# Kernel tuning notes

Measured on AMD Instinct MI355X. Metric: run time of the kernel, lower is better.

The kernel has to match this reference:

```python
import jax, jax.numpy as jnp
import numpy as np

# SectorAttention (PARTNER): dim=256, resolution=(4,4096), H_sp=4, W_sp=1, H=4, heads=8
B, Hq, Hres, Wres, C, NH = 4, 4, 4, 4096, 256, 8
H_SP, W_SP = 4, 1
HD = C // NH
SCALE = HD ** -0.5


def _forward(s, x, s_pos, x_pos, Wq, bq, Wk, bk, Wv, bv, Wo, bo,
             pw1, pb1, bn_g, bn_b, bn_m, bn_v, pw2, pb2,
             ln_g, ln_b, mw1, mb1, mw2, mb2):
    Bb, Lq, Cc = s.shape
    W = Wres
    nW = Bb * (W // W_SP)
    # ---- dynamic relative-position bias (per-window small conv net) ----
    xp = x_pos.reshape(Bb, Hq // H_SP, H_SP, W // W_SP, W_SP, 2)
    xp = jnp.transpose(xp, (0, 1, 3, 5, 2, 4)).reshape(-1, 2, H_SP * W_SP)   # (nW,2,4)
    sp = jnp.transpose(s_pos, (0, 2, 3, 1)).reshape(-1, 2, Hq * W_SP)        # (nW,2,4)
    rel = sp[:, :, :, None] - xp[:, :, None, :]                              # (nW,2,4,4)
    rel = rel.reshape(nW, 2, -1)                                             # (nW,2,16)
    h = jnp.einsum('oc,bcl->bol', pw1, rel) + pb1[None, :, None]             # Conv1d k=1
    h = (h - bn_m[None, :, None]) * jax.lax.rsqrt(bn_v[None, :, None] + 1e-5) \
        * bn_g[None, :, None] + bn_b[None, :, None]                          # BatchNorm1d (eval)
    h = jax.nn.relu(h)
    h = jnp.einsum('oc,bcl->bol', pw2, h) + pb2[None, :, None]               # Conv1d k=1 -> heads
    rel_bias = h.reshape(-1, NH, Hq, H_SP)                                   # (nW,NH,4,4) since W_SP==1
    # ---- projections + window partitioning ----
    q = s @ Wq.T + bq
    q = q.reshape(Bb, Cc, Hq, W)                          # faithful torch .view reinterpretation
    q = q.reshape(Bb, NH, HD, Hq, W // W_SP, W_SP)
    q = jnp.transpose(q, (0, 4, 1, 3, 5, 2)).reshape(-1, NH, Hq * W_SP, HD)

    def im2cswin(t):
        t = jnp.transpose(t, (0, 2, 1)).reshape(Bb, Cc, Hres, W)
        t = t.reshape(Bb, Cc, Hres // H_SP, H_SP, W // W_SP, W_SP)
        t = jnp.transpose(t, (0, 2, 4, 3, 5, 1)).reshape(-1, H_SP * W_SP, Cc)
        return jnp.transpose(t.reshape(-1, H_SP * W_SP, NH, HD), (0, 2, 1, 3))

    k = im2cswin(x @ Wk.T + bk)
    v = im2cswin(x @ Wv.T + bv)
    # ---- windowed attention with dynamic bias ----
    attn = jnp.einsum('wnqd,wnkd->wnqk', q * SCALE, k) + rel_bias
    attn = jax.nn.softmax(attn, axis=-1)
    o = jnp.einsum('wnqk,wnkd->wnqd', attn, v)            # (nW,NH,4,HD)
    o = jnp.transpose(o, (0, 2, 1, 3)).reshape(-1, Hq * W_SP, Cc)
    # windows2img(o, H_sp=Hq, W_sp=W_SP, H=Hq, W=W)
    o = o.reshape(Bb, Hq // Hq, W // W_SP, Hq, W_SP, Cc)
    o = jnp.transpose(o, (0, 1, 3, 2, 4, 5)).reshape(Bb, Hq * W, Cc)
    o = o @ Wo.T + bo
    s1 = s + o
    # ---- LayerNorm + MLP (residual) ----
    mu = jnp.mean(s1, axis=-1, keepdims=True)
    var = jnp.mean((s1 - mu) ** 2, axis=-1, keepdims=True)
    n = (s1 - mu) * jax.lax.rsqrt(var + 1e-5) * ln_g + ln_b
    h2 = jax.nn.gelu(n @ mw1.T + mb1, approximate=False)
    return s1 + h2 @ mw2.T + mb2


def setup_inputs() -> dict:
    key = jax.random.key(0)
    ks = jax.random.split(key, 12)
    rn = lambda k, sh, sc=1.0: jax.random.normal(k, sh, dtype=jnp.float32) * sc
    H4 = 4 * C
    return {
        's': rn(ks[0], (B, Hq * Wres, C)),
        'x': rn(ks[1], (B, Hres * Wres, C)),
        's_pos': rn(ks[2], (B, 2, Wres // W_SP, Hq * W_SP)),
        'x_pos': rn(ks[3], (B, Hres * Wres, 2)),
        'Wq': rn(ks[4], (C, C), 0.02), 'bq': jnp.zeros((C,), jnp.float32),
        'Wk': rn(ks[5], (C, C), 0.02), 'bk': jnp.zeros((C,), jnp.float32),
        'Wv': rn(ks[6], (C, C), 0.02), 'bv': jnp.zeros((C,), jnp.float32),
        'Wo': rn(ks[7], (C, C), 0.02), 'bo': jnp.zeros((C,), jnp.float32),
        'pw1': rn(ks[8], (16, 2), 0.2), 'pb1': jnp.zeros((16,), jnp.float32),
        'bn_g': jnp.ones((16,), jnp.float32), 'bn_b': jnp.zeros((16,), jnp.float32),
        'bn_m': jnp.zeros((16,), jnp.float32), 'bn_v': jnp.ones((16,), jnp.float32),
        'pw2': rn(ks[9], (NH, 16), 0.2), 'pb2': jnp.zeros((NH,), jnp.float32),
        'ln_g': jnp.ones((C,), jnp.float32), 'ln_b': jnp.zeros((C,), jnp.float32),
        'mw1': rn(ks[10], (H4, C), 0.02), 'mb1': jnp.zeros((H4,), jnp.float32),
        'mw2': rn(ks[11], (C, H4), 0.02), 'mb2': jnp.zeros((C,), jnp.float32),
    }


def reference(s, x, s_pos, x_pos, Wq, bq, Wk, bk, Wv, bv, Wo, bo,
              pw1, pb1, bn_g, bn_b, bn_m, bn_v, pw2, pb2,
              ln_g, ln_b, mw1, mb1, mw2, mb2):
    return _forward(s, x, s_pos, x_pos, Wq, bq, Wk, bk, Wv, bv, Wo, bo,
                    pw1, pb1, bn_g, bn_b, bn_m, bn_v, pw2, pb2,
                    ln_g, ln_b, mw1, mb1, mw2, mb2)
```

## Files before the change

### kernel.cpp

```cpp
#include <hip/hip_runtime.h>
#include <hip/hip_bf16.h>
#include <math.h>

typedef __hip_bfloat16 BF;
typedef __bf16 bf16x8 __attribute__((ext_vector_type(8)));
typedef float f32x4 __attribute__((ext_vector_type(4)));

struct alignas(8) BF4 { BF v[4]; };
struct alignas(16) BF8 { BF v[8]; };

static __device__ __forceinline__ float b2f(BF x) { return __bfloat162float(x); }
static __device__ __forceinline__ BF f2b(float x) { return __float2bfloat16(x); }

static __device__ __forceinline__ void gld_lds16(const void* g, void* l) {
  __builtin_amdgcn_global_load_lds(
      (const __attribute__((address_space(1))) unsigned int*)g,
      (__attribute__((address_space(3))) unsigned int*)l, 16, 0, 0);
}

__global__ void __launch_bounds__(256) cvt_kernel(
    const float* __restrict__ in, BF* __restrict__ out, int n4) {
  for (int i = blockIdx.x * 256 + threadIdx.x; i < n4; i += gridDim.x * 256) {
    float4 v = ((const float4*)in)[i];
    BF4 o;
    o.v[0] = f2b(v.x); o.v[1] = f2b(v.y); o.v[2] = f2b(v.z); o.v[3] = f2b(v.w);
    ((BF4*)out)[i] = o;
  }
}

__global__ void __launch_bounds__(256) bkv_kernel(
    const float* __restrict__ bk, const float* __restrict__ bv,
    float* __restrict__ bkv) {
  int i = blockIdx.x * 256 + threadIdx.x;
  bkv[i] = (i < 256) ? bk[i] : bv[i - 256];
}

__global__ void __launch_bounds__(256) bias_kernel(
    const float* __restrict__ s_pos, const float* __restrict__ x_pos,
    const float* __restrict__ pw1, const float* __restrict__ pb1,
    const float* __restrict__ bn_g, const float* __restrict__ bn_b,
    const float* __restrict__ bn_m, const float* __restrict__ bn_v,
    const float* __restrict__ pw2, const float* __restrict__ pb2,
    float* __restrict__ out) {
  int gid = blockIdx.x * 256 + threadIdx.x;
  int w = gid >> 4, l = gid & 15;
  int b = w >> 12, wi = w & 4095;
  int i = l >> 2, j = l & 3;
  int e0 = i, e1 = 4 + i;
  float sp0 = s_pos[(((size_t)b * 2 + (e0 & 1)) * 4096 + wi) * 4 + (e0 >> 1)];
  float sp1 = s_pos[(((size_t)b * 2 + (e1 & 1)) * 4096 + wi) * 4 + (e1 >> 1)];
  float xp0 = x_pos[((size_t)b * 16384 + j * 4096 + wi) * 2 + 0];
  float xp1 = x_pos[((size_t)b * 16384 + j * 4096 + wi) * 2 + 1];
  float r0 = sp0 - xp0, r1 = sp1 - xp1;
  float acc[8];
#pragma unroll
  for (int p = 0; p < 8; ++p) acc[p] = pb2[p];
#pragma unroll
  for (int o = 0; o < 16; ++o) {
    float t = pw1[o * 2 + 0] * r0 + pw1[o * 2 + 1] * r1 + pb1[o];
    float sc = bn_g[o] / sqrtf(bn_v[o] + 1e-5f);
    t = (t - bn_m[o]) * sc + bn_b[o];
    t = fmaxf(t, 0.0f);
#pragma unroll
    for (int p = 0; p < 8; ++p) acc[p] += pw2[p * 16 + o] * t;
  }
#pragma unroll
  for (int p = 0; p < 8; ++p) out[(size_t)w * 128 + p * 16 + l] = acc[p];
}

enum { EPI_NONE = 0, EPI_RES = 1, EPI_GELU = 2 };

template <int EPI, typename AT, typename RT, typename CT>
__global__ void __launch_bounds__(256, 4) gemm_tn(
    const AT* __restrict__ A, const BF* __restrict__ Bw,
    const float* __restrict__ bias, const RT* __restrict__ Res,
    CT* __restrict__ C, int M, int N, int K) {
  constexpr bool F32A = __is_same(AT, float);
  alignas(16) __shared__ BF As[8][128][8];
  alignas(16) __shared__ BF Bs[8][128][8];
  const int ntiles = N >> 7;
  const int cpx = gridDim.x >> 3;
  const int bid = blockIdx.x;
  const int swz = (bid & 7) * cpx + (bid >> 3);
  const int mt = swz / ntiles, nt = swz % ntiles;
  const int row0 = mt << 7, col0 = nt << 7;
  const int t = threadIdx.x;
  const int wave = t >> 6, lane = t & 63;
  const int wr = wave >> 1, wc = wave & 1;
  const int sm = t & 127;
  const int skc = t >> 7;
  f32x4 acc[4][4] = {};
  const int NT = K >> 6;
  float4 ar[4][2];

  auto stageB = [&](int kt) {
#pragma unroll
    for (int i = 0; i < 4; ++i) {
      const int kc = i * 2 + skc;
      gld_lds16(Bw + (size_t)(col0 + sm) * K + kt * 64 + kc * 8,
                &Bs[0][0][0] + (size_t)(i * 256 + wave * 64) * 8);
    }
  };
  auto loadA = [&](int kt) {
    if constexpr (F32A) {
#pragma unroll
      for (int i = 0; i < 4; ++i) {
        const int kc = i * 2 + skc;
        const float* src = A + (size_t)(row0 + sm) * K + kt * 64 + kc * 8;
        ar[i][0] = ((const float4*)src)[0];
        ar[i][1] = ((const float4*)src)[1];
      }
    }
  };
  auto writeA = [&]() {
    if constexpr (F32A) {
#pragma unroll
      for (int i = 0; i < 4; ++i) {
        const int kc = i * 2 + skc;
        BF tmp[8];
        tmp[0] = f2b(ar[i][0].x); tmp[1] = f2b(ar[i][0].y);
        tmp[2] = f2b(ar[i][0].z); tmp[3] = f2b(ar[i][0].w);
        tmp[4] = f2b(ar[i][1].x); tmp[5] = f2b(ar[i][1].y);
        tmp[6] = f2b(ar[i][1].z); tmp[7] = f2b(ar[i][1].w);
        *(bf16x8*)(&As[kc][sm][0]) = *(bf16x8*)tmp;
      }
    }
  };
  auto stageA_bf = [&](int kt) {
    if constexpr (!F32A) {
#pragma unroll
      for (int i = 0; i < 4; ++i) {
        const int kc = i * 2 + skc;
        gld_lds16((const BF*)A + (size_t)(row0 + sm) * K + kt * 64 + kc * 8,
                  &As[0][0][0] + (size_t)(i * 256 + wave * 64) * 8);
      }
    }
  };
  auto compute = [&]() {
#pragma unroll
    for (int kk = 0; kk < 2; ++kk) {
      const int chunk = kk * 4 + (lane >> 4);
      const int rl = lane & 15;
      bf16x8 af[4], bfr[4];
#pragma unroll
      for (int mi = 0; mi < 4; ++mi)
        af[mi] = *(const bf16x8*)(&As[chunk][wr * 64 + mi * 16 + rl][0]);
#pragma unroll
      for (int ni = 0; ni < 4; ++ni)
        bfr[ni] = *(const bf16x8*)(&Bs[chunk][wc * 64 + ni * 16 + rl][0]);
#pragma unroll
      for (int mi = 0; mi < 4; ++mi)
#pragma unroll
        for (int ni = 0; ni < 4; ++ni)
          acc[mi][ni] = __builtin_amdgcn_mfma_f32_16x16x32_bf16(
              af[mi], bfr[ni], acc[mi][ni], 0, 0, 0);
    }
  };

  loadA(0);
  for (int kt = 0; kt < NT; ++kt) {
    writeA();
    stageA_bf(kt);
    stageB(kt);
    if (kt + 1 < NT) loadA(kt + 1);
    __syncthreads();
    compute();
    __syncthreads();
  }

  const int rl = lane & 15, rg = lane >> 4;
#pragma unroll
  for (int mi = 0; mi < 4; ++mi) {
#pragma unroll
    for (int ni = 0; ni < 4; ++ni) {
      const int col = col0 + wc * 64 + ni * 16 + rl;
      const float bcol = bias[col];
#pragma unroll
      for (int r = 0; r < 4; ++r) {
        const int row = row0 + wr * 64 + mi * 16 + rg * 4 + r;
        float v = acc[mi][ni][r] + bcol;
        if constexpr (EPI == EPI_GELU)
          v = 0.5f * v * (1.0f + erff(v * 0.70710678118654752f));
        if constexpr (EPI == EPI_RES) {
          if constexpr (__is_same(RT, float))
            v += Res[(size_t)row * N + col];
          else
            v += b2f(Res[(size_t)row * N + col]);
        }
        if constexpr (__is_same(CT, float))
          C[(size_t)row * N + col] = v;
        else
          C[(size_t)row * N + col] = f2b(v);
      }
    }
  }
}

__global__ void __launch_bounds__(256, 4) gemm_q(
    const float* __restrict__ A, const BF* __restrict__ Bw,
    const float* __restrict__ bias, BF* __restrict__ Qa) {
  constexpr int K = 256;
  alignas(16) __shared__ BF As[8][128][8];
  alignas(16) __shared__ BF Bs[8][128][8];
  const int cpx = gridDim.x >> 3;
  const int bid = blockIdx.x;
  const int swz = (bid & 7) * cpx + (bid >> 3);
  const int mt = swz >> 1, nt = swz & 1;
  const int hp = mt & 3, qi = (mt >> 2) & 3, nh = (mt >> 4) & 7, bb = mt >> 7;
  const int col0 = nt << 7;
  const int t = threadIdx.x;
  const int wave = t >> 6, lane = t & 63;
  const int wr = wave >> 1, wc = wave & 1;
  const int sm = t & 127;
  const int skc = t >> 7;
  const size_t grow = (size_t)bb * 16384 + nh * 2048 + (size_t)(sm & 31) * 64 +
                      qi * 16 + hp * 4 + (sm >> 5);
  f32x4 acc[4][4] = {};
  float4 ar[4][2];

  auto stageB = [&](int kt) {
#pragma unroll
    for (int i = 0; i < 4; ++i) {
      const int kc = i * 2 + skc;
      gld_lds16(Bw + (size_t)(col0 + sm) * K + kt * 64 + kc * 8,
                &Bs[0][0][0] + (size_t)(i * 256 + wave * 64) * 8);
    }
  };
  auto loadA = [&](int kt) {
#pragma unroll
    for (int i = 0; i < 4; ++i) {
      const int kc = i * 2 + skc;
      const float* src = A + grow * K + kt * 64 + kc * 8;
      ar[i][0] = ((const float4*)src)[0];
      ar[i][1] = ((const float4*)src)[1];
    }
  };
  auto writeA = [&]() {
#pragma unroll
    for (int i = 0; i < 4; ++i) {
      const int kc = i * 2 + skc;
      BF tmp[8];
      tmp[0] = f2b(ar[i][0].x); tmp[1] = f2b(ar[i][0].y);
      tmp[2] = f2b(ar[i][0].z); tmp[3] = f2b(ar[i][0].w);
      tmp[4] = f2b(ar[i][1].x); tmp[5] = f2b(ar[i][1].y);
      tmp[6] = f2b(ar[i][1].z); tmp[7] = f2b(ar[i][1].w);
      *(bf16x8*)(&As[kc][sm][0]) = *(bf16x8*)tmp;
    }
  };
  auto compute = [&]() {
#pragma unroll
    for (int kk = 0; kk < 2; ++kk) {
      const int chunk = kk * 4 + (lane >> 4);
      const int rl = lane & 15;
      bf16x8 af[4], bfr[4];
#pragma unroll
      for (int mi = 0; mi < 4; ++mi)
        af[mi] = *(const bf16x8*)(&As[chunk][wr * 64 + mi * 16 + rl][0]);
#pragma unroll
      for (int ni = 0; ni < 4; ++ni)
        bfr[ni] = *(const bf16x8*)(&Bs[chunk][wc * 64 + ni * 16 + rl][0]);
#pragma unroll
      for (int mi = 0; mi < 4; ++mi)
#pragma unroll
        for (int ni = 0; ni < 4; ++ni)
          acc[mi][ni] = __builtin_amdgcn_mfma_f32_16x16x32_bf16(
              af[mi], bfr[ni], acc[mi][ni], 0, 0, 0);
    }
  };

  loadA(0);
  for (int kt = 0; kt < 4; ++kt) {
    writeA();
    stageB(kt);
    if (kt + 1 < 4) loadA(kt + 1);
    __syncthreads();
    compute();
    __syncthreads();
  }

  const int rl = lane & 15, rg = lane >> 4;
  const float SCALE = 0.17677669529663689f;
#pragma unroll
  for (int mi = 0; mi < 4; ++mi) {
#pragma unroll
    for (int ni = 0; ni < 4; ++ni) {
      const int col = col0 + wc * 64 + ni * 16 + rl;
      const float bcol = bias[col];
      const int i0 = wr * 64 + mi * 16 + rg * 4;
      const int hd = i0 & 31, hil = i0 >> 5;
      const int wi = (hp * 4 + hil) * 256 + col;
      BF4 pk;
#pragma unroll
      for (int r = 0; r < 4; ++r)
        pk.v[r] = f2b((acc[mi][ni][r] + bcol) * SCALE);
      *(BF4*)(Qa + ((((size_t)bb * 4096 + wi) * 8 + nh) * 128 + qi * 32 + hd)) = pk;
    }
  }
}

__global__ void __launch_bounds__(256) attn_kernel(
    const BF* __restrict__ Qa, const BF* __restrict__ KV,
    const float* __restrict__ biasb, BF* __restrict__ O) {
  const int t = threadIdx.x;
  const int g = t >> 4, l16 = t & 15;
  const int qi = l16 >> 2, kj = l16 & 3;
  const int w = (blockIdx.x << 1) | (g >> 3);
  const int nh = g & 7;
  const int b = w >> 12, wi = w & 4095;

  const uint4* qp = (const uint4*)(Qa + ((((size_t)b * 4096 + wi) * 8 + nh) * 128 + qi * 32));
  uint4 qv[4] = {qp[0], qp[1], qp[2], qp[3]};
  const uint4* kp = (const uint4*)(KV + ((size_t)b * 16384 + kj * 4096 + wi) * 512 + nh * 32);
  uint4 kv[4] = {kp[0], kp[1], kp[2], kp[3]};
  const float bias_l = biasb[(size_t)w * 128 + nh * 16 + l16];
  const BF* vbase = KV + (size_t)b * 16384 * 512 + 256 + nh * 32 + kj * 8;
  uint4 vv[4];
#pragma unroll
  for (int d = 0; d < 4; ++d)
    vv[d] = *(const uint4*)(vbase + ((size_t)((kj ^ d) * 4096 + wi)) * 512);

  float accs[4] = {0.f, 0.f, 0.f, 0.f};
#pragma unroll
  for (int j = 0; j < 4; ++j) {
#pragma unroll
    for (int e = 0; e < 4; ++e) {
      unsigned qe = ((const unsigned*)&qv[j])[e];
      unsigned ke = ((const unsigned*)&kv[j])[e];
      float ql = __uint_as_float(qe << 16);
      float qh = __uint_as_float(qe & 0xffff0000u);
      float kl = __uint_as_float(ke << 16);
      float kh = __uint_as_float(ke & 0xffff0000u);
      accs[e] = fmaf(ql, kl, accs[e]);
      accs[e] = fmaf(qh, kh, accs[e]);
    }
  }
  const float score = accs[0] + accs[1] + accs[2] + accs[3] + bias_l;

  float mx = fmaxf(score, __shfl_xor(score, 1));
  mx = fmaxf(mx, __shfl_xor(mx, 2));
  float e = __expf(score - mx);
  float sm = e + __shfl_xor(e, 1);
  sm += __shfl_xor(sm, 2);
  float p = e / sm;
  float pd[4];
  pd[0] = p;
  pd[1] = __shfl_xor(p, 1);
  pd[2] = __shfl_xor(p, 2);
  pd[3] = __shfl_xor(pd[1], 2);

  float o8[8] = {0.f, 0.f, 0.f, 0.f, 0.f, 0.f, 0.f, 0.f};
#pragma unroll
  for (int d = 0; d < 4; ++d) {
#pragma unroll
    for (int e2 = 0; e2 < 4; ++e2) {
      unsigned ve = ((const unsigned*)&vv[d])[e2];
      o8[e2 * 2 + 0] = fmaf(pd[d], __uint_as_float(ve << 16), o8[e2 * 2 + 0]);
      o8[e2 * 2 + 1] = fmaf(pd[d], __uint_as_float(ve & 0xffff0000u), o8[e2 * 2 + 1]);
    }
  }
  BF8 ob;
#pragma unroll
  for (int h = 0; h < 8; ++h) ob.v[h] = f2b(o8[h]);
  *(BF8*)(O + ((size_t)b * 16384 + qi * 4096 + wi) * 256 + nh * 32 + kj * 8) = ob;
}

__global__ void __launch_bounds__(256) ln_kernel(
    const BF* __restrict__ S1, const float* __restrict__ g,
    const float* __restrict__ be, BF* __restrict__ Nout) {
  const int wave = threadIdx.x >> 6, lane = threadIdx.x & 63;
  const size_t row = (size_t)blockIdx.x * 4 + wave;
  BF4 d = *(const BF4*)(S1 + row * 256 + lane * 4);
  float x[4] = {b2f(d.v[0]), b2f(d.v[1]), b2f(d.v[2]), b2f(d.v[3])};
  float s = x[0] + x[1] + x[2] + x[3];
  float sq = x[0] * x[0] + x[1] * x[1] + x[2] * x[2] + x[3] * x[3];
#pragma unroll
  for (int m = 1; m <= 32; m <<= 1) {
    s += __shfl_xor(s, m);
    sq += __shfl_xor(sq, m);
  }
  const float mean = s * 0.00390625f;
  const float var = sq * 0.00390625f - mean * mean;
  const float rstd = 1.0f / sqrtf(var + 1e-5f);
  BF4 o;
#pragma unroll
  for (int jj = 0; jj < 4; ++jj) {
    float nv = (x[jj] - mean) * rstd * g[lane * 4 + jj] + be[lane * 4 + jj];
    o.v[jj] = f2b(nv);
  }
  *(BF4*)(Nout + row * 256 + lane * 4) = o;
}

extern "C" void kernel_launch(void* const* d_in, const int* in_sizes, int n_in,
                              void* d_out, int out_size, void* d_ws, size_t ws_size,
                              hipStream_t stream) {
  const float* s     = (const float*)d_in[0];
  const float* x     = (const float*)d_in[1];
  const float* s_pos = (const float*)d_in[2];
  const float* x_pos = (const float*)d_in[3];
  const float* Wq = (const float*)d_in[4];  const float* bq = (const float*)d_in[5];
  const float* Wk = (const float*)d_in[6];  const float* bk = (const float*)d_in[7];
  const float* Wv = (const float*)d_in[8];  const float* bv = (const float*)d_in[9];
  const float* Wo = (const float*)d_in[10]; const float* bo = (const float*)d_in[11];
  const float* pw1 = (const float*)d_in[12]; const float* pb1 = (const float*)d_in[13];
  const float* bn_g = (const float*)d_in[14]; const float* bn_b = (const float*)d_in[15];
  const float* bn_m = (const float*)d_in[16]; const float* bn_v = (const float*)d_in[17];
  const float* pw2 = (const float*)d_in[18]; const float* pb2 = (const float*)d_in[19];
  const float* ln_g = (const float*)d_in[20]; const float* ln_b = (const float*)d_in[21];
  const float* mw1 = (const float*)d_in[22]; const float* mb1 = (const float*)d_in[23];
  const float* mw2 = (const float*)d_in[24]; const float* mb2 = (const float*)d_in[25];

  char* ws = (char*)d_ws;
  float* biasb = (float*)ws;
  BF* Qa   = (BF*)(ws + 8388608);
  BF* KVw  = (BF*)(ws + 41943040);
  BF* S1   = (BF*)(ws + 109051904);
  BF* Wq_bf  = (BF*)(ws + 142606336);
  BF* Wo_bf  = (BF*)(ws + 142737408);
  BF* Wkv_bf = (BF*)(ws + 142868480);
  BF* mw1_bf = (BF*)(ws + 143130624);
  BF* mw2_bf = (BF*)(ws + 143654912);
  float* bkv = (float*)(ws + 144179200);
  BF* Nw = Qa;
  BF* H2 = KVw;
  BF* ObBF = (BF*)d_out;
  float* Of = (float*)d_out;

  cvt_kernel<<<64, 256, 0, stream>>>(Wq, Wq_bf, 16384);
  cvt_kernel<<<64, 256, 0, stream>>>(Wo, Wo_bf, 16384);
  cvt_kernel<<<64, 256, 0, stream>>>(Wk, Wkv_bf, 16384);
  cvt_kernel<<<64, 256, 0, stream>>>(Wv, Wkv_bf + 65536, 16384);
  cvt_kernel<<<256, 256, 0, stream>>>(mw1, mw1_bf, 65536);
  cvt_kernel<<<256, 256, 0, stream>>>(mw2, mw2_bf, 65536);
  bkv_kernel<<<2, 256, 0, stream>>>(bk, bv, bkv);
  bias_kernel<<<1024, 256, 0, stream>>>(s_pos, x_pos, pw1, pb1, bn_g, bn_b,
                                        bn_m, bn_v, pw2, pb2, biasb);

  gemm_q<<<1024, 256, 0, stream>>>(s, Wq_bf, bq, Qa);
  gemm_tn<EPI_NONE, float, float, BF><<<2048, 256, 0, stream>>>(
      x, Wkv_bf, bkv, nullptr, KVw, 65536, 512, 256);
  attn_kernel<<<8192, 256, 0, stream>>>(Qa, KVw, biasb, ObBF);
  gemm_tn<EPI_RES, BF, float, BF><<<1024, 256, 0, stream>>>(
      ObBF, Wo_bf, bo, s, S1, 65536, 256, 256);
  ln_kernel<<<16384, 256, 0, stream>>>(S1, ln_g, ln_b, Nw);
  for (int h = 0; h < 2; ++h) {
    const size_t ro = (size_t)h * 32768;
    gemm_tn<EPI_GELU, BF, float, BF><<<2048, 256, 0, stream>>>(
        Nw + ro * 256, mw1_bf, mb1, nullptr, H2, 32768, 1024, 256);
    gemm_tn<EPI_RES, BF, BF, float><<<512, 256, 0, stream>>>(
        H2, mw2_bf, mb2, S1 + ro * 256, Of + ro * 256, 32768, 256, 1024);
  }
}
```

Measured before the change: 408.4 us.

## Fuse weight conversion, bias net, and LayerNorm into consuming GEMM and attention kernels

Drops the separate weight fp32-to-bf16 conversion kernels. GEMMs now read fp32 weights and convert them in registers before writing to LDS, instead of using direct global-to-LDS loads of bf16. The relative-position bias MLP is recomputed inside the attention kernel rather than stored and reloaded, and LayerNorm is fused into a new MLP1 kernel that keeps a normalized 128-row A tile in LDS and loops over all eight N tiles. This removes about ten launches and several intermediate buffers. In exchange, weights are reloaded and converted at fp32 width in every block, the direct LDS loads are lost, and the fused MLP1 kernel runs at lower occupancy (256 blocks, 2 per CU) with no overlap of B-tile staging and compute.

```diff
diff --git a/kernel.cpp b/kernel.cpp
--- a/kernel.cpp
+++ b/kernel.cpp
@@ -18,62 +18,13 @@
       (__attribute__((address_space(3))) unsigned int*)l, 16, 0, 0);
 }
 
-__global__ void __launch_bounds__(256) cvt_kernel(
-    const float* __restrict__ in, BF* __restrict__ out, int n4) {
-  for (int i = blockIdx.x * 256 + threadIdx.x; i < n4; i += gridDim.x * 256) {
-    float4 v = ((const float4*)in)[i];
-    BF4 o;
-    o.v[0] = f2b(v.x); o.v[1] = f2b(v.y); o.v[2] = f2b(v.z); o.v[3] = f2b(v.w);
-    ((BF4*)out)[i] = o;
-  }
-}
-
-__global__ void __launch_bounds__(256) bkv_kernel(
-    const float* __restrict__ bk, const float* __restrict__ bv,
-    float* __restrict__ bkv) {
-  int i = blockIdx.x * 256 + threadIdx.x;
-  bkv[i] = (i < 256) ? bk[i] : bv[i - 256];
-}
-
-__global__ void __launch_bounds__(256) bias_kernel(
-    const float* __restrict__ s_pos, const float* __restrict__ x_pos,
-    const float* __restrict__ pw1, const float* __restrict__ pb1,
-    const float* __restrict__ bn_g, const float* __restrict__ bn_b,
-    const float* __restrict__ bn_m, const float* __restrict__ bn_v,
-    const float* __restrict__ pw2, const float* __restrict__ pb2,
-    float* __restrict__ out) {
-  int gid = blockIdx.x * 256 + threadIdx.x;
-  int w = gid >> 4, l = gid & 15;
-  int b = w >> 12, wi = w & 4095;
-  int i = l >> 2, j = l & 3;
-  int e0 = i, e1 = 4 + i;
-  float sp0 = s_pos[(((size_t)b * 2 + (e0 & 1)) * 4096 + wi) * 4 + (e0 >> 1)];
-  float sp1 = s_pos[(((size_t)b * 2 + (e1 & 1)) * 4096 + wi) * 4 + (e1 >> 1)];
-  float xp0 = x_pos[((size_t)b * 16384 + j * 4096 + wi) * 2 + 0];
-  float xp1 = x_pos[((size_t)b * 16384 + j * 4096 + wi) * 2 + 1];
-  float r0 = sp0 - xp0, r1 = sp1 - xp1;
-  float acc[8];
-#pragma unroll
-  for (int p = 0; p < 8; ++p) acc[p] = pb2[p];
-#pragma unroll
-  for (int o = 0; o < 16; ++o) {
-    float t = pw1[o * 2 + 0] * r0 + pw1[o * 2 + 1] * r1 + pb1[o];
-    float sc = bn_g[o] / sqrtf(bn_v[o] + 1e-5f);
-    t = (t - bn_m[o]) * sc + bn_b[o];
-    t = fmaxf(t, 0.0f);
-#pragma unroll
-    for (int p = 0; p < 8; ++p) acc[p] += pw2[p * 16 + o] * t;
-  }
-#pragma unroll
-  for (int p = 0; p < 8; ++p) out[(size_t)w * 128 + p * 16 + l] = acc[p];
-}
-
 enum { EPI_NONE = 0, EPI_RES = 1, EPI_GELU = 2 };
 
-template <int EPI, typename AT, typename RT, typename CT>
+template <int EPI, bool DUALB, typename AT, typename RT, typename CT>
 __global__ void __launch_bounds__(256, 4) gemm_tn(
-    const AT* __restrict__ A, const BF* __restrict__ Bw,
-    const float* __restrict__ bias, const RT* __restrict__ Res,
+    const AT* __restrict__ A, const float* __restrict__ B1,
+    const float* __restrict__ B2, const float* __restrict__ bias1,
+    const float* __restrict__ bias2, const RT* __restrict__ Res,
     CT* __restrict__ C, int M, int N, int K) {
   constexpr bool F32A = __is_same(AT, float);
   alignas(16) __shared__ BF As[8][128][8];
@@ -93,12 +44,24 @@
   const int NT = K >> 6;
   float4 ar[4][2];
 
+  const int brow = col0 + sm;
+  const float* bptr;
+  if constexpr (DUALB)
+    bptr = (brow < 256) ? (B1 + (size_t)brow * K) : (B2 + (size_t)(brow - 256) * K);
+  else
+    bptr = B1 + (size_t)brow * K;
+
   auto stageB = [&](int kt) {
 #pragma unroll
     for (int i = 0; i < 4; ++i) {
       const int kc = i * 2 + skc;
-      gld_lds16(Bw + (size_t)(col0 + sm) * K + kt * 64 + kc * 8,
-                &Bs[0][0][0] + (size_t)(i * 256 + wave * 64) * 8);
+      const float* src = bptr + kt * 64 + kc * 8;
+      float4 b0 = ((const float4*)src)[0];
+      float4 b1 = ((const float4*)src)[1];
+      BF tmp[8];
+      tmp[0] = f2b(b0.x); tmp[1] = f2b(b0.y); tmp[2] = f2b(b0.z); tmp[3] = f2b(b0.w);
+      tmp[4] = f2b(b1.x); tmp[5] = f2b(b1.y); tmp[6] = f2b(b1.z); tmp[7] = f2b(b1.w);
+      *(bf16x8*)(&Bs[kc][sm][0]) = *(bf16x8*)tmp;
     }
   };
   auto loadA = [&](int kt) {
@@ -174,7 +137,11 @@
 #pragma unroll
     for (int ni = 0; ni < 4; ++ni) {
       const int col = col0 + wc * 64 + ni * 16 + rl;
-      const float bcol = bias[col];
+      float bcol;
+      if constexpr (DUALB)
+        bcol = (col < 256) ? bias1[col] : bias2[col - 256];
+      else
+        bcol = bias1[col];
 #pragma unroll
       for (int r = 0; r < 4; ++r) {
         const int row = row0 + wr * 64 + mi * 16 + rg * 4 + r;
@@ -197,7 +164,7 @@
 }
 
 __global__ void __launch_bounds__(256, 4) gemm_q(
-    const float* __restrict__ A, const BF* __restrict__ Bw,
+    const float* __restrict__ A, const float* __restrict__ Bw,
     const float* __restrict__ bias, BF* __restrict__ Qa) {
   constexpr int K = 256;
   alignas(16) __shared__ BF As[8][128][8];
@@ -215,6 +182,7 @@
   const int skc = t >> 7;
   const size_t grow = (size_t)bb * 16384 + nh * 2048 + (size_t)(sm & 31) * 64 +
                       qi * 16 + hp * 4 + (sm >> 5);
+  const float* bptr = Bw + (size_t)(col0 + sm) * K;
   f32x4 acc[4][4] = {};
   float4 ar[4][2];
 
@@ -222,8 +190,13 @@
 #pragma unroll
     for (int i = 0; i < 4; ++i) {
       const int kc = i * 2 + skc;
-      gld_lds16(Bw + (size_t)(col0 + sm) * K + kt * 64 + kc * 8,
-                &Bs[0][0][0] + (size_t)(i * 256 + wave * 64) * 8);
+      const float* src = bptr + kt * 64 + kc * 8;
+      float4 b0 = ((const float4*)src)[0];
+      float4 b1 = ((const float4*)src)[1];
+      BF tmp[8];
+      tmp[0] = f2b(b0.x); tmp[1] = f2b(b0.y); tmp[2] = f2b(b0.z); tmp[3] = f2b(b0.w);
+      tmp[4] = f2b(b1.x); tmp[5] = f2b(b1.y); tmp[6] = f2b(b1.z); tmp[7] = f2b(b1.w);
+      *(bf16x8*)(&Bs[kc][sm][0]) = *(bf16x8*)tmp;
     }
   };
   auto loadA = [&](int kt) {
@@ -298,9 +271,133 @@
   }
 }
 
+__global__ void __launch_bounds__(256, 2) gemm_mlp1ln(
+    const BF* __restrict__ S1p, const float* __restrict__ mw1,
+    const float* __restrict__ mb1, const float* __restrict__ ln_g,
+    const float* __restrict__ ln_b, BF* __restrict__ H2) {
+  constexpr int K = 256, N = 1024;
+  alignas(16) __shared__ BF As[4][8][128][8];
+  alignas(16) __shared__ BF Bs[8][128][8];
+  const int cpx = gridDim.x >> 3;
+  const int bid = blockIdx.x;
+  const int mt = (bid & 7) * cpx + (bid >> 3);
+  const int row0 = mt << 7;
+  const int t = threadIdx.x;
+  const int wave = t >> 6, lane = t & 63;
+  const int wr = wave >> 1, wc = wave & 1;
+
+#pragma unroll
+  for (int kt = 0; kt < 4; ++kt)
+#pragma unroll
+    for (int i = 0; i < 4; ++i) {
+      const int e = i * 256 + t;
+      const int kc = e >> 7, m = e & 127;
+      gld_lds16(S1p + (size_t)(row0 + m) * K + kt * 64 + kc * 8,
+                &As[kt][0][0][0] + (size_t)(i * 256 + wave * 64) * 8);
+    }
+  __syncthreads();
+
+  {
+    const int row = t >> 1, half = t & 1;
+    float s = 0.f, sq = 0.f;
+    bf16x8 vv[16];
+#pragma unroll
+    for (int j = 0; j < 16; ++j) {
+      const int kt = half * 2 + (j >> 3), kc = j & 7;
+      vv[j] = *(const bf16x8*)(&As[kt][kc][row][0]);
+#pragma unroll
+      for (int e = 0; e < 8; ++e) {
+        float x = (float)vv[j][e];
+        s += x; sq += x * x;
+      }
+    }
+    s += __shfl_xor(s, 1);
+    sq += __shfl_xor(sq, 1);
+    const float mean = s * 0.00390625f;
+    const float var = sq * 0.00390625f - mean * mean;
+    const float rstd = 1.0f / sqrtf(var + 1e-5f);
+#pragma unroll
+    for (int j = 0; j < 16; ++j) {
+      const int kt = half * 2 + (j >> 3), kc = j & 7;
+      const int k0 = kt * 64 + kc * 8;
+      float4 g0 = *(const float4*)(ln_g + k0);
+      float4 g1 = *(const float4*)(ln_g + k0 + 4);
+      float4 c0 = *(const float4*)(ln_b + k0);
+      float4 c1 = *(const float4*)(ln_b + k0 + 4);
+      float gg[8] = {g0.x, g0.y, g0.z, g0.w, g1.x, g1.y, g1.z, g1.w};
+      float cc[8] = {c0.x, c0.y, c0.z, c0.w, c1.x, c1.y, c1.z, c1.w};
+      BF tmp[8];
+#pragma unroll
+      for (int e = 0; e < 8; ++e)
+        tmp[e] = f2b(((float)vv[j][e] - mean) * rstd * gg[e] + cc[e]);
+      *(bf16x8*)(&As[kt][kc][row][0]) = *(bf16x8*)tmp;
+    }
+  }
+  __syncthreads();
+
+  const int sm = t & 127, skc = t >> 7;
+  const int rl = lane & 15, rg = lane >> 4;
+  for (int nt = 0; nt < 8; ++nt) {
+    const int col0 = nt << 7;
+    const float* bptr = mw1 + (size_t)(col0 + sm) * K;
+    f32x4 acc[4][4] = {};
+    for (int kt = 0; kt < 4; ++kt) {
+#pragma unroll
+      for (int i = 0; i < 4; ++i) {
+        const int kc = i * 2 + skc;
+        const float* src = bptr + kt * 64 + kc * 8;
+        float4 b0 = ((const float4*)src)[0];
+        float4 b1 = ((const float4*)src)[1];
+        BF tmp[8];
+        tmp[0] = f2b(b0.x); tmp[1] = f2b(b0.y); tmp[2] = f2b(b0.z); tmp[3] = f2b(b0.w);
+        tmp[4] = f2b(b1.x); tmp[5] = f2b(b1.y); tmp[6] = f2b(b1.z); tmp[7] = f2b(b1.w);
+        *(bf16x8*)(&Bs[kc][sm][0]) = *(bf16x8*)tmp;
+      }
+      __syncthreads();
+#pragma unroll
+      for (int kk = 0; kk < 2; ++kk) {
+        const int chunk = kk * 4 + (lane >> 4);
+        bf16x8 af[4], bfr[4];
+#pragma unroll
+        for (int mi = 0; mi < 4; ++mi)
+          af[mi] = *(const bf16x8*)(&As[kt][chunk][wr * 64 + mi * 16 + rl][0]);
+#pragma unroll
+        for (int ni = 0; ni < 4; ++ni)
+          bfr[ni] = *(const bf16x8*)(&Bs[chunk][wc * 64 + ni * 16 + rl][0]);
+#pragma unroll
+        for (int mi = 0; mi < 4; ++mi)
+#pragma unroll
+          for (int ni = 0; ni < 4; ++ni)
+            acc[mi][ni] = __builtin_amdgcn_mfma_f32_16x16x32_bf16(
+                af[mi], bfr[ni], acc[mi][ni], 0, 0, 0);
+      }
+      __syncthreads();
+    }
+#pragma unroll
+    for (int mi = 0; mi < 4; ++mi)
+#pragma unroll
+      for (int ni = 0; ni < 4; ++ni) {
+        const int col = col0 + wc * 64 + ni * 16 + rl;
+        const float bcol = mb1[col];
+#pragma unroll
+        for (int r = 0; r < 4; ++r) {
+          const int row = row0 + wr * 64 + mi * 16 + rg * 4 + r;
+          float v = acc[mi][ni][r] + bcol;
+          v = 0.5f * v * (1.0f + erff(v * 0.70710678118654752f));
+          H2[(size_t)row * N + col] = f2b(v);
+        }
+      }
+  }
+}
+
 __global__ void __launch_bounds__(256) attn_kernel(
     const BF* __restrict__ Qa, const BF* __restrict__ KV,
-    const float* __restrict__ biasb, BF* __restrict__ O) {
+    const float* __restrict__ s_pos, const float* __restrict__ x_pos,
+    const float* __restrict__ pw1, const float* __restrict__ pb1,
+    const float* __restrict__ bn_g, const float* __restrict__ bn_b,
+    const float* __restrict__ bn_m, const float* __restrict__ bn_v,
+    const float* __restrict__ pw2, const float* __restrict__ pb2,
+    BF* __restrict__ O) {
   const int t = threadIdx.x;
   const int g = t >> 4, l16 = t & 15;
   const int qi = l16 >> 2, kj = l16 & 3;
@@ -312,12 +409,25 @@
   uint4 qv[4] = {qp[0], qp[1], qp[2], qp[3]};
   const uint4* kp = (const uint4*)(KV + ((size_t)b * 16384 + kj * 4096 + wi) * 512 + nh * 32);
   uint4 kv[4] = {kp[0], kp[1], kp[2], kp[3]};
-  const float bias_l = biasb[(size_t)w * 128 + nh * 16 + l16];
   const BF* vbase = KV + (size_t)b * 16384 * 512 + 256 + nh * 32 + kj * 8;
   uint4 vv[4];
 #pragma unroll
   for (int d = 0; d < 4; ++d)
     vv[d] = *(const uint4*)(vbase + ((size_t)((kj ^ d) * 4096 + wi)) * 512);
+
+  const size_t sprow = ((size_t)(b * 2 + (qi & 1)) * 4096 + wi) * 4;
+  const float r0 = s_pos[sprow + (qi >> 1)] -
+                   x_pos[((size_t)b * 16384 + kj * 4096 + wi) * 2 + 0];
+  const float r1 = s_pos[sprow + 2 + (qi >> 1)] -
+                   x_pos[((size_t)b * 16384 + kj * 4096 + wi) * 2 + 1];
+  float bias_l = pb2[nh];
+#pragma unroll
+  for (int o = 0; o < 16; ++o) {
+    float tv = pw1[o * 2 + 0] * r0 + pw1[o * 2 + 1] * r1 + pb1[o];
+    const float sc = bn_g[o] / sqrtf(bn_v[o] + 1e-5f);
+    tv = (tv - bn_m[o]) * sc + bn_b[o];
+    bias_l += pw2[nh * 16 + o] * fmaxf(tv, 0.0f);
+  }
 
   float accs[4] = {0.f, 0.f, 0.f, 0.f};
 #pragma unroll
@@ -362,32 +472,6 @@
 #pragma unroll
   for (int h = 0; h < 8; ++h) ob.v[h] = f2b(o8[h]);
   *(BF8*)(O + ((size_t)b * 16384 + qi * 4096 + wi) * 256 + nh * 32 + kj * 8) = ob;
-}
-
-__global__ void __launch_bounds__(256) ln_kernel(
-    const BF* __restrict__ S1, const float* __restrict__ g,
-    const float* __restrict__ be, BF* __restrict__ Nout) {
-  const int wave = threadIdx.x >> 6, lane = threadIdx.x & 63;
-  const size_t row = (size_t)blockIdx.x * 4 + wave;
-  BF4 d = *(const BF4*)(S1 + row * 256 + lane * 4);
-  float x[4] = {b2f(d.v[0]), b2f(d.v[1]), b2f(d.v[2]), b2f(d.v[3])};
-  float s = x[0] + x[1] + x[2] + x[3];
-  float sq = x[0] * x[0] + x[1] * x[1] + x[2] * x[2] + x[3] * x[3];
-#pragma unroll
-  for (int m = 1; m <= 32; m <<= 1) {
-    s += __shfl_xor(s, m);
-    sq += __shfl_xor(sq, m);
-  }
-  const float mean = s * 0.00390625f;
-  const float var = sq * 0.00390625f - mean * mean;
-  const float rstd = 1.0f / sqrtf(var + 1e-5f);
-  BF4 o;
-#pragma unroll
-  for (int jj = 0; jj < 4; ++jj) {
-    float nv = (x[jj] - mean) * rstd * g[lane * 4 + jj] + be[lane * 4 + jj];
-    o.v[jj] = f2b(nv);
-  }
-  *(BF4*)(Nout + row * 256 + lane * 4) = o;
 }
 
 extern "C" void kernel_launch(void* const* d_in, const int* in_sizes, int n_in,
@@ -410,43 +494,25 @@
   const float* mw2 = (const float*)d_in[24]; const float* mb2 = (const float*)d_in[25];
 
   char* ws = (char*)d_ws;
-  float* biasb = (float*)ws;
-  BF* Qa   = (BF*)(ws + 8388608);
-  BF* KVw  = (BF*)(ws + 41943040);
-  BF* S1   = (BF*)(ws + 109051904);
-  BF* Wq_bf  = (BF*)(ws + 142606336);
-  BF* Wo_bf  = (BF*)(ws + 142737408);
-  BF* Wkv_bf = (BF*)(ws + 142868480);
-  BF* mw1_bf = (BF*)(ws + 143130624);
-  BF* mw2_bf = (BF*)(ws + 143654912);
-  float* bkv = (float*)(ws + 144179200);
-  BF* Nw = Qa;
+  BF* Qa  = (BF*)(ws);
+  BF* KVw = (BF*)(ws + 33554432);
+  BF* S1  = (BF*)(ws + 100663296);
   BF* H2 = KVw;
   BF* ObBF = (BF*)d_out;
   float* Of = (float*)d_out;
 
-  cvt_kernel<<<64, 256, 0, stream>>>(Wq, Wq_bf, 16384);
-  cvt_kernel<<<64, 256, 0, stream>>>(Wo, Wo_bf, 16384);
-  cvt_kernel<<<64, 256, 0, stream>>>(Wk, Wkv_bf, 16384);
-  cvt_kernel<<<64, 256, 0, stream>>>(Wv, Wkv_bf + 65536, 16384);
-  cvt_kernel<<<256, 256, 0, stream>>>(mw1, mw1_bf, 65536);
-  cvt_kernel<<<256, 256, 0, stream>>>(mw2, mw2_bf, 65536);
-  bkv_kernel<<<2, 256, 0, stream>>>(bk, bv, bkv);
-  bias_kernel<<<1024, 256, 0, stream>>>(s_pos, x_pos, pw1, pb1, bn_g, bn_b,
-                                        bn_m, bn_v, pw2, pb2, biasb);
-
-  gemm_q<<<1024, 256, 0, stream>>>(s, Wq_bf, bq, Qa);
-  gemm_tn<EPI_NONE, float, float, BF><<<2048, 256, 0, stream>>>(
-      x, Wkv_bf, bkv, nullptr, KVw, 65536, 512, 256);
-  attn_kernel<<<8192, 256, 0, stream>>>(Qa, KVw, biasb, ObBF);
-  gemm_tn<EPI_RES, BF, float, BF><<<1024, 256, 0, stream>>>(
-      ObBF, Wo_bf, bo, s, S1, 65536, 256, 256);
-  ln_kernel<<<16384, 256, 0, stream>>>(S1, ln_g, ln_b, Nw);
+  gemm_q<<<1024, 256, 0, stream>>>(s, Wq, bq, Qa);
+  gemm_tn<EPI_NONE, true, float, float, BF><<<2048, 256, 0, stream>>>(
+      x, Wk, Wv, bk, bv, nullptr, KVw, 65536, 512, 256);
+  attn_kernel<<<8192, 256, 0, stream>>>(Qa, KVw, s_pos, x_pos, pw1, pb1,
+                                        bn_g, bn_b, bn_m, bn_v, pw2, pb2, ObBF);
+  gemm_tn<EPI_RES, false, BF, float, BF><<<1024, 256, 0, stream>>>(
+      ObBF, Wo, nullptr, bo, nullptr, s, S1, 65536, 256, 256);
   for (int h = 0; h < 2; ++h) {
     const size_t ro = (size_t)h * 32768;
-    gemm_tn<EPI_GELU, BF, float, BF><<<2048, 256, 0, stream>>>(
-        Nw + ro * 256, mw1_bf, mb1, nullptr, H2, 32768, 1024, 256);
-    gemm_tn<EPI_RES, BF, BF, float><<<512, 256, 0, stream>>>(
-        H2, mw2_bf, mb2, S1 + ro * 256, Of + ro * 256, 32768, 256, 1024);
+    gemm_mlp1ln<<<256, 256, 0, stream>>>(S1 + ro * 256, mw1, mb1, ln_g, ln_b, H2);
+    gemm_tn<EPI_RES, false, BF, BF, float><<<512, 256, 0, stream>>>(
+        H2, mw2, nullptr, mb2, nullptr, S1 + ro * 256, Of + ro * 256,
+        32768, 256, 1024);
   }
 }
```

Measured after the change: 568.4 us. 1.39x slower.

## Fuse relative-position bias into attention and widen GEMM tiles to 128x256

Applied to the files above, without the earlier changes.

The separate bias kernel and its workspace buffer are removed. Each attention thread now recomputes its own position-bias scalar from s_pos/x_pos with the small conv/BN/ReLU network. Separately, all GEMMs move from 256-thread 128x128 tiles to 512-thread 128x256 tiles with 8 waves, halving grid sizes and reusing each A tile across twice as many columns. The cost is more LDS per block and fewer blocks, and the GEMM index remapping must stay correct for every shape.

```diff
diff --git a/kernel.cpp b/kernel.cpp
--- a/kernel.cpp
+++ b/kernel.cpp
@@ -35,77 +35,56 @@
   bkv[i] = (i < 256) ? bk[i] : bv[i - 256];
 }
 
-__global__ void __launch_bounds__(256) bias_kernel(
-    const float* __restrict__ s_pos, const float* __restrict__ x_pos,
-    const float* __restrict__ pw1, const float* __restrict__ pb1,
-    const float* __restrict__ bn_g, const float* __restrict__ bn_b,
-    const float* __restrict__ bn_m, const float* __restrict__ bn_v,
-    const float* __restrict__ pw2, const float* __restrict__ pb2,
-    float* __restrict__ out) {
-  int gid = blockIdx.x * 256 + threadIdx.x;
-  int w = gid >> 4, l = gid & 15;
-  int b = w >> 12, wi = w & 4095;
-  int i = l >> 2, j = l & 3;
-  int e0 = i, e1 = 4 + i;
-  float sp0 = s_pos[(((size_t)b * 2 + (e0 & 1)) * 4096 + wi) * 4 + (e0 >> 1)];
-  float sp1 = s_pos[(((size_t)b * 2 + (e1 & 1)) * 4096 + wi) * 4 + (e1 >> 1)];
-  float xp0 = x_pos[((size_t)b * 16384 + j * 4096 + wi) * 2 + 0];
-  float xp1 = x_pos[((size_t)b * 16384 + j * 4096 + wi) * 2 + 1];
-  float r0 = sp0 - xp0, r1 = sp1 - xp1;
-  float acc[8];
-#pragma unroll
-  for (int p = 0; p < 8; ++p) acc[p] = pb2[p];
-#pragma unroll
-  for (int o = 0; o < 16; ++o) {
-    float t = pw1[o * 2 + 0] * r0 + pw1[o * 2 + 1] * r1 + pb1[o];
-    float sc = bn_g[o] / sqrtf(bn_v[o] + 1e-5f);
-    t = (t - bn_m[o]) * sc + bn_b[o];
-    t = fmaxf(t, 0.0f);
-#pragma unroll
-    for (int p = 0; p < 8; ++p) acc[p] += pw2[p * 16 + o] * t;
-  }
-#pragma unroll
-  for (int p = 0; p < 8; ++p) out[(size_t)w * 128 + p * 16 + l] = acc[p];
-}
-
 enum { EPI_NONE = 0, EPI_RES = 1, EPI_GELU = 2 };
 
 template <int EPI, typename AT, typename RT, typename CT>
-__global__ void __launch_bounds__(256, 4) gemm_tn(
+__global__ void __launch_bounds__(512, 4) gemm_tn(
     const AT* __restrict__ A, const BF* __restrict__ Bw,
     const float* __restrict__ bias, const RT* __restrict__ Res,
     CT* __restrict__ C, int M, int N, int K) {
   constexpr bool F32A = __is_same(AT, float);
   alignas(16) __shared__ BF As[8][128][8];
-  alignas(16) __shared__ BF Bs[8][128][8];
-  const int ntiles = N >> 7;
+  alignas(16) __shared__ BF Bs[8][256][8];
+  const int ntiles = N >> 8;
   const int cpx = gridDim.x >> 3;
   const int bid = blockIdx.x;
   const int swz = (bid & 7) * cpx + (bid >> 3);
   const int mt = swz / ntiles, nt = swz % ntiles;
-  const int row0 = mt << 7, col0 = nt << 7;
+  const int row0 = mt << 7, col0 = nt << 8;
   const int t = threadIdx.x;
   const int wave = t >> 6, lane = t & 63;
-  const int wr = wave >> 1, wc = wave & 1;
+  const int wr = wave >> 2, wc = wave & 3;
   const int sm = t & 127;
   const int skc = t >> 7;
   f32x4 acc[4][4] = {};
   const int NT = K >> 6;
-  float4 ar[4][2];
+  float4 ar[2][2];
 
   auto stageB = [&](int kt) {
 #pragma unroll
     for (int i = 0; i < 4; ++i) {
-      const int kc = i * 2 + skc;
-      gld_lds16(Bw + (size_t)(col0 + sm) * K + kt * 64 + kc * 8,
-                &Bs[0][0][0] + (size_t)(i * 256 + wave * 64) * 8);
+      const int c = i * 512 + t;
+      const int kc = c >> 8, n = c & 255;
+      gld_lds16(Bw + (size_t)(col0 + n) * K + kt * 64 + kc * 8,
+                &Bs[0][0][0] + (size_t)(i * 512 + wave * 64) * 8);
+    }
+  };
+  auto stageA_bf = [&](int kt) {
+    if constexpr (!F32A) {
+#pragma unroll
+      for (int i = 0; i < 2; ++i) {
+        const int c = i * 512 + t;
+        const int kc = c >> 7, m = c & 127;
+        gld_lds16((const BF*)A + (size_t)(row0 + m) * K + kt * 64 + kc * 8,
+                  &As[0][0][0] + (size_t)(i * 512 + wave * 64) * 8);
+      }
     }
   };
   auto loadA = [&](int kt) {
     if constexpr (F32A) {
 #pragma unroll
-      for (int i = 0; i < 4; ++i) {
-        const int kc = i * 2 + skc;
+      for (int i = 0; i < 2; ++i) {
+        const int kc = i * 4 + skc;
         const float* src = A + (size_t)(row0 + sm) * K + kt * 64 + kc * 8;
         ar[i][0] = ((const float4*)src)[0];
         ar[i][1] = ((const float4*)src)[1];
@@ -115,24 +94,14 @@
   auto writeA = [&]() {
     if constexpr (F32A) {
 #pragma unroll
-      for (int i = 0; i < 4; ++i) {
-        const int kc = i * 2 + skc;
+      for (int i = 0; i < 2; ++i) {
+        const int kc = i * 4 + skc;
         BF tmp[8];
         tmp[0] = f2b(ar[i][0].x); tmp[1] = f2b(ar[i][0].y);
         tmp[2] = f2b(ar[i][0].z); tmp[3] = f2b(ar[i][0].w);
         tmp[4] = f2b(ar[i][1].x); tmp[5] = f2b(ar[i][1].y);
         tmp[6] = f2b(ar[i][1].z); tmp[7] = f2b(ar[i][1].w);
         *(bf16x8*)(&As[kc][sm][0]) = *(bf16x8*)tmp;
-      }
-    }
-  };
-  auto stageA_bf = [&](int kt) {
-    if constexpr (!F32A) {
-#pragma unroll
-      for (int i = 0; i < 4; ++i) {
-        const int kc = i * 2 + skc;
-        gld_lds16((const BF*)A + (size_t)(row0 + sm) * K + kt * 64 + kc * 8,
-                  &As[0][0][0] + (size_t)(i * 256 + wave * 64) * 8);
       }
     }
   };
@@ -196,40 +165,39 @@
   }
 }
 
-__global__ void __launch_bounds__(256, 4) gemm_q(
+__global__ void __launch_bounds__(512, 4) gemm_q(
     const float* __restrict__ A, const BF* __restrict__ Bw,
     const float* __restrict__ bias, BF* __restrict__ Qa) {
   constexpr int K = 256;
   alignas(16) __shared__ BF As[8][128][8];
-  alignas(16) __shared__ BF Bs[8][128][8];
+  alignas(16) __shared__ BF Bs[8][256][8];
   const int cpx = gridDim.x >> 3;
   const int bid = blockIdx.x;
-  const int swz = (bid & 7) * cpx + (bid >> 3);
-  const int mt = swz >> 1, nt = swz & 1;
+  const int mt = (bid & 7) * cpx + (bid >> 3);
   const int hp = mt & 3, qi = (mt >> 2) & 3, nh = (mt >> 4) & 7, bb = mt >> 7;
-  const int col0 = nt << 7;
   const int t = threadIdx.x;
   const int wave = t >> 6, lane = t & 63;
-  const int wr = wave >> 1, wc = wave & 1;
+  const int wr = wave >> 2, wc = wave & 3;
   const int sm = t & 127;
   const int skc = t >> 7;
   const size_t grow = (size_t)bb * 16384 + nh * 2048 + (size_t)(sm & 31) * 64 +
                       qi * 16 + hp * 4 + (sm >> 5);
   f32x4 acc[4][4] = {};
-  float4 ar[4][2];
+  float4 ar[2][2];
 
   auto stageB = [&](int kt) {
 #pragma unroll
     for (int i = 0; i < 4; ++i) {
-      const int kc = i * 2 + skc;
-      gld_lds16(Bw + (size_t)(col0 + sm) * K + kt * 64 + kc * 8,
-                &Bs[0][0][0] + (size_t)(i * 256 + wave * 64) * 8);
+      const int c = i * 512 + t;
+      const int kc = c >> 8, n = c & 255;
+      gld_lds16(Bw + (size_t)n * K + kt * 64 + kc * 8,
+                &Bs[0][0][0] + (size_t)(i * 512 + wave * 64) * 8);
     }
   };
   auto loadA = [&](int kt) {
 #pragma unroll
-    for (int i = 0; i < 4; ++i) {
-      const int kc = i * 2 + skc;
+    for (int i = 0; i < 2; ++i) {
+      const int kc = i * 4 + skc;
       const float* src = A + grow * K + kt * 64 + kc * 8;
       ar[i][0] = ((const float4*)src)[0];
       ar[i][1] = ((const float4*)src)[1];
@@ -237,8 +205,8 @@
   };
   auto writeA = [&]() {
 #pragma unroll
-    for (int i = 0; i < 4; ++i) {
-      const int kc = i * 2 + skc;
+    for (int i = 0; i < 2; ++i) {
+      const int kc = i * 4 + skc;
       BF tmp[8];
       tmp[0] = f2b(ar[i][0].x); tmp[1] = f2b(ar[i][0].y);
       tmp[2] = f2b(ar[i][0].z); tmp[3] = f2b(ar[i][0].w);
@@ -284,7 +252,7 @@
   for (int mi = 0; mi < 4; ++mi) {
 #pragma unroll
     for (int ni = 0; ni < 4; ++ni) {
-      const int col = col0 + wc * 64 + ni * 16 + rl;
+      const int col = wc * 64 + ni * 16 + rl;
       const float bcol = bias[col];
       const int i0 = wr * 64 + mi * 16 + rg * 4;
       const int hd = i0 & 31, hil = i0 >> 5;
@@ -300,7 +268,12 @@
 
 __global__ void __launch_bounds__(256) attn_kernel(
     const BF* __restrict__ Qa, const BF* __restrict__ KV,
-    const float* __restrict__ biasb, BF* __restrict__ O) {
+    const float* __restrict__ s_pos, const float* __restrict__ x_pos,
+    const float* __restrict__ pw1, const float* __restrict__ pb1,
+    const float* __restrict__ bn_g, const float* __restrict__ bn_b,
+    const float* __restrict__ bn_m, const float* __restrict__ bn_v,
+    const float* __restrict__ pw2, const float* __restrict__ pb2,
+    BF* __restrict__ O) {
   const int t = threadIdx.x;
   const int g = t >> 4, l16 = t & 15;
   const int qi = l16 >> 2, kj = l16 & 3;
@@ -312,12 +285,25 @@
   uint4 qv[4] = {qp[0], qp[1], qp[2], qp[3]};
   const uint4* kp = (const uint4*)(KV + ((size_t)b * 16384 + kj * 4096 + wi) * 512 + nh * 32);
   uint4 kv[4] = {kp[0], kp[1], kp[2], kp[3]};
-  const float bias_l = biasb[(size_t)w * 128 + nh * 16 + l16];
   const BF* vbase = KV + (size_t)b * 16384 * 512 + 256 + nh * 32 + kj * 8;
   uint4 vv[4];
 #pragma unroll
   for (int d = 0; d < 4; ++d)
     vv[d] = *(const uint4*)(vbase + ((size_t)((kj ^ d) * 4096 + wi)) * 512);
+
+  const size_t sprow = ((size_t)(b * 2 + (qi & 1)) * 4096 + wi) * 4;
+  const float r0 = s_pos[sprow + (qi >> 1)] -
+                   x_pos[((size_t)b * 16384 + kj * 4096 + wi) * 2 + 0];
+  const float r1 = s_pos[sprow + 2 + (qi >> 1)] -
+                   x_pos[((size_t)b * 16384 + kj * 4096 + wi) * 2 + 1];
+  float bias_l = pb2[nh];
+#pragma unroll
+  for (int o = 0; o < 16; ++o) {
+    float tv = pw1[o * 2 + 0] * r0 + pw1[o * 2 + 1] * r1 + pb1[o];
+    const float sc = bn_g[o] / sqrtf(bn_v[o] + 1e-5f);
+    tv = (tv - bn_m[o]) * sc + bn_b[o];
+    bias_l += pw2[nh * 16 + o] * fmaxf(tv, 0.0f);
+  }
 
   float accs[4] = {0.f, 0.f, 0.f, 0.f};
 #pragma unroll
@@ -410,7 +396,6 @@
   const float* mw2 = (const float*)d_in[24]; const float* mb2 = (const float*)d_in[25];
 
   char* ws = (char*)d_ws;
-  float* biasb = (float*)ws;
   BF* Qa   = (BF*)(ws + 8388608);
   BF* KVw  = (BF*)(ws + 41943040);
   BF* S1   = (BF*)(ws + 109051904);
@@ -432,21 +417,20 @@
   cvt_kernel<<<256, 256, 0, stream>>>(mw1, mw1_bf, 65536);
   cvt_kernel<<<256, 256, 0, stream>>>(mw2, mw2_bf, 65536);
   bkv_kernel<<<2, 256, 0, stream>>>(bk, bv, bkv);
-  bias_kernel<<<1024, 256, 0, stream>>>(s_pos, x_pos, pw1, pb1, bn_g, bn_b,
-                                        bn_m, bn_v, pw2, pb2, biasb);
-
-  gemm_q<<<1024, 256, 0, stream>>>(s, Wq_bf, bq, Qa);
-  gemm_tn<EPI_NONE, float, float, BF><<<2048, 256, 0, stream>>>(
+
+  gemm_q<<<512, 512, 0, stream>>>(s, Wq_bf, bq, Qa);
+  gemm_tn<EPI_NONE, float, float, BF><<<1024, 512, 0, stream>>>(
       x, Wkv_bf, bkv, nullptr, KVw, 65536, 512, 256);
-  attn_kernel<<<8192, 256, 0, stream>>>(Qa, KVw, biasb, ObBF);
-  gemm_tn<EPI_RES, BF, float, BF><<<1024, 256, 0, stream>>>(
+  attn_kernel<<<8192, 256, 0, stream>>>(Qa, KVw, s_pos, x_pos, pw1, pb1,
+                                        bn_g, bn_b, bn_m, bn_v, pw2, pb2, ObBF);
+  gemm_tn<EPI_RES, BF, float, BF><<<512, 512, 0, stream>>>(
       ObBF, Wo_bf, bo, s, S1, 65536, 256, 256);
   ln_kernel<<<16384, 256, 0, stream>>>(S1, ln_g, ln_b, Nw);
   for (int h = 0; h < 2; ++h) {
     const size_t ro = (size_t)h * 32768;
-    gemm_tn<EPI_GELU, BF, float, BF><<<2048, 256, 0, stream>>>(
+    gemm_tn<EPI_GELU, BF, BF, BF><<<1024, 512, 0, stream>>>(
         Nw + ro * 256, mw1_bf, mb1, nullptr, H2, 32768, 1024, 256);
-    gemm_tn<EPI_RES, BF, BF, float><<<512, 256, 0, stream>>>(
+    gemm_tn<EPI_RES, BF, BF, float><<<256, 512, 0, stream>>>(
         H2, mw2_bf, mb2, S1 + ro * 256, Of + ro * 256, 32768, 256, 1024);
   }
 }
```

Measured after the change: 428.1 us. 1.05x slower.
